# Optimization experiments

Hardware: AMD Instinct MI355X
Metric: run time of the kernel (lower is better)

The kernel has to match this reference:

```python
import jax, jax.numpy as jnp
import numpy as np

B, L, E, H = 4, 4096, 1024, 16
HD = E // H
I = 4096  # intermediate_size = 4*E
RMS_EPS = 1e-6
ATTN_EPS = 1e-6
GATE_INIT = 0.1  # 0.1 + 0.05*layer_idx, layer_idx=0


def rmsnorm(x, w, eps=RMS_EPS):
    xf = x.astype(jnp.float32)
    var = jnp.mean(xf * xf, axis=-1, keepdims=True)
    return w * (xf * jax.lax.rsqrt(var + eps)).astype(x.dtype)


def rotate_half(x):
    d = x.shape[-1] // 2
    return jnp.concatenate([-x[..., d:], x[..., :d]], axis=-1)


def setup_inputs() -> dict:
    key = jax.random.key(0)
    ks = jax.random.split(key, 16)
    h = jax.random.normal(ks[0], (B, L, E), jnp.float32)
    c = jax.random.normal(ks[1], (B, E), jnp.float32)
    # standard RoPE tables, shape (L, HD)
    pos = jnp.arange(L, dtype=jnp.float32)
    inv = 1.0 / (10000.0 ** (jnp.arange(0, HD, 2, dtype=jnp.float32) / HD))
    fr = pos[:, None] * inv[None, :]
    emb = jnp.concatenate([fr, fr], axis=-1)
    cos, sin = jnp.cos(emb), jnp.sin(emb)
    s = 0.02
    Wq = jax.random.normal(ks[2], (E, E), jnp.float32) * s
    Wk = jax.random.normal(ks[3], (E, E), jnp.float32) * s
    Wv = jax.random.normal(ks[4], (E, E), jnp.float32) * s
    Wo = jax.random.normal(ks[5], (E, E), jnp.float32) * s
    Wg = jax.random.normal(ks[6], (I, E), jnp.float32) * s
    Wu = jax.random.normal(ks[7], (I, E), jnp.float32) * s
    Wd = jax.random.normal(ks[8], (E, I), jnp.float32) * s
    w_norm1 = jnp.ones((E,), jnp.float32)
    w_norm2 = jnp.ones((E,), jnp.float32)
    Wada = jax.random.normal(ks[9], (6 * E, E), jnp.float32) * 0.01
    bada = np.zeros((6 * E,), np.float32)
    bada[2 * E:3 * E] = GATE_INIT  # gate_msa
    bada[5 * E:6 * E] = GATE_INIT  # gate_mlp
    bada = jnp.asarray(bada)
    return {"h": h, "c": c, "cos": cos, "sin": sin, "Wq": Wq, "Wk": Wk,
            "Wv": Wv, "Wo": Wo, "Wg": Wg, "Wu": Wu, "Wd": Wd,
            "w_norm1": w_norm1, "w_norm2": w_norm2, "Wada": Wada, "bada": bada}


def reference(h, c, cos, sin, Wq, Wk, Wv, Wo, Wg, Wu, Wd, w_norm1, w_norm2, Wada, bada):
    # adaLN modulation: (B, 6E) -> six (B,1,E) chunks
    mod = c @ Wada.T + bada
    sh1, sc1, g1, sh2, sc2, g2 = [m[:, None, :] for m in jnp.split(mod, 6, axis=-1)]

    # --- attention branch ---
    x = rmsnorm(h, w_norm1) * (1.0 + sc1) + sh1  # modulate
    q = jax.nn.silu(x @ Wq.T).reshape(B, L, H, HD).transpose(0, 2, 1, 3)  # (B,H,L,hd)
    k = jax.nn.silu(x @ Wk.T).reshape(B, L, H, HD).transpose(0, 2, 1, 3)
    v = (x @ Wv.T).reshape(B, L, H, HD).transpose(0, 2, 1, 3)
    cs = cos[None, None]  # (1,1,L,hd)
    sn = sin[None, None]
    q = q * cs + rotate_half(q) * sn
    k = k * cs + rotate_half(k) * sn
    # cosFormer sin/cos feature map; m = max(src,tgt) = L
    idx = (np.pi / 2) * jnp.arange(1, L + 1, dtype=jnp.float32) / L  # (L,)
    sw = jnp.sin(idx)[None, None, :, None]
    cw = jnp.cos(idx)[None, None, :, None]
    q_ = jnp.concatenate([q * sw, q * cw], axis=-1)  # (B,H,L,2hd)
    k_ = jnp.concatenate([k * sw, k * cw], axis=-1)
    # non-causal linear attention: K^T V first (O(L))
    kv = jnp.einsum('bhld,bhlm->bhdm', k_, v)             # (B,H,2hd,hd)
    z = 1.0 / jnp.maximum(jnp.einsum('bhld,bhd->bhl', q_, k_.sum(axis=2)), ATTN_EPS)
    attn = jnp.einsum('bhld,bhdm,bhl->bhlm', q_, kv, z)   # (B,H,L,hd)
    attn = attn.transpose(0, 2, 1, 3).reshape(B, L, E) @ Wo.T
    h = h + g1 * attn  # bias_dropout_add_scale, eval mode

    # --- MLP branch ---
    x = rmsnorm(h, w_norm2) * (1.0 + sc2) + sh2
    mlp = (jax.nn.silu(x @ Wg.T) * (x @ Wu.T)) @ Wd.T
    return h + g2 * mlp
```

## Files before the change

### kernel.cpp

```cpp
#include <hip/hip_runtime.h>
#include <hip/hip_bf16.h>

#define BB 4
#define LL 4096
#define EE 1024
#define HH 16
#define II 4096
#define MM (BB*LL)

using f32x4 = __attribute__((ext_vector_type(4))) float;
using s16x8 = __attribute__((ext_vector_type(8))) short;
using u32x4 = __attribute__((ext_vector_type(4))) unsigned int;

__device__ __forceinline__ unsigned short f2bf(float f) {
  union { float f; unsigned u; } x; x.f = f;
  unsigned r = x.u + 0x7fffu + ((x.u >> 16) & 1u);
  return (unsigned short)(r >> 16);
}
__device__ __forceinline__ float bf2f(unsigned short s) {
  union { unsigned u; float f; } x; x.u = ((unsigned)s) << 16;
  return x.f;
}
__device__ __forceinline__ unsigned packbf(float lo, float hi) {
  return ((unsigned)f2bf(hi) << 16) | (unsigned)f2bf(lo);
}
__device__ __forceinline__ float silu_f(float x) { return x / (1.0f + expf(-x)); }

__device__ __forceinline__ void gll16(const void* g, void* l) {
  __builtin_amdgcn_global_load_lds(
      (const __attribute__((address_space(1))) unsigned int*)g,
      (__attribute__((address_space(3))) unsigned int*)l, 16, 0, 0);
}

__global__ __launch_bounds__(256) void k_mod(const float* __restrict__ c,
    const float* __restrict__ Wada, const float* __restrict__ bada,
    float* __restrict__ mod) {
  __shared__ float cs[EE];
  int b = blockIdx.y;
  int n = blockIdx.x * 256 + threadIdx.x;
  for (int i = threadIdx.x; i < EE; i += 256) cs[i] = c[b*EE + i];
  __syncthreads();
  const float4* wp = (const float4*)(Wada + (size_t)n * EE);
  float acc = 0.f;
  for (int k = 0; k < EE/4; k++) {
    float4 t = wp[k];
    acc += t.x*cs[4*k] + t.y*cs[4*k+1] + t.z*cs[4*k+2] + t.w*cs[4*k+3];
  }
  mod[(size_t)b*6*EE + n] = acc + bada[n];
}

__global__ __launch_bounds__(256) void k_coef(const float* __restrict__ mod,
    const float* __restrict__ w1, const float* __restrict__ w2,
    float* __restrict__ cf1, float* __restrict__ cf2) {
  int k = blockIdx.x * 256 + threadIdx.x;
  int b = blockIdx.y;
  const float* mb = mod + (size_t)b*6*EE;
  cf1[(size_t)b*2048 + k]        = w1[k] * (1.0f + mb[EE + k]);
  cf1[(size_t)b*2048 + 1024 + k] = mb[k];
  cf2[(size_t)b*2048 + k]        = w2[k] * (1.0f + mb[4*EE + k]);
  cf2[(size_t)b*2048 + 1024 + k] = mb[3*EE + k];
}

__global__ __launch_bounds__(256) void k_rsig(const float* __restrict__ in,
    float* __restrict__ rsig) {
  int row = blockIdx.x;
  int t = threadIdx.x;
  float4 v = ((const float4*)(in + (size_t)row * EE))[t];
  float ss = v.x*v.x + v.y*v.y + v.z*v.z + v.w*v.w;
  #pragma unroll
  for (int o = 32; o > 0; o >>= 1) ss += __shfl_down(ss, o, 64);
  __shared__ float red[4];
  if ((t & 63) == 0) red[t >> 6] = ss;
  __syncthreads();
  float tot = red[0] + red[1] + red[2] + red[3];
  if (t == 0) rsig[row] = 1.0f / sqrtf(tot * (1.0f/1024.0f) + 1e-6f);
}

__global__ __launch_bounds__(256) void k_f2b(const float* __restrict__ s,
    unsigned short* __restrict__ d, int n4) {
  int i = blockIdx.x * 256 + threadIdx.x;
  if (i >= n4) return;
  float4 v = ((const float4*)s)[i];
  ushort4 u; u.x = f2bf(v.x); u.y = f2bf(v.y); u.z = f2bf(v.z); u.w = f2bf(v.w);
  ((ushort4*)d)[i] = u;
}

__global__ __launch_bounds__(256) void k_split1(const float* __restrict__ h,
    const float* __restrict__ rsig, const float* __restrict__ cf,
    unsigned short* __restrict__ xh, unsigned short* __restrict__ xl) {
  int row = blockIdx.x;
  int t = threadIdx.x;
  int b = row >> 12;
  float rs = rsig[row];
  const float* cfb = cf + (size_t)b*2048;
  float4 v  = ((const float4*)(h + (size_t)row*EE))[t];
  float4 c1 = ((const float4*)cfb)[t];
  float4 c0 = ((const float4*)(cfb + 1024))[t];
  float x0 = fmaf(v.x*rs, c1.x, c0.x);
  float x1 = fmaf(v.y*rs, c1.y, c0.y);
  float x2 = fmaf(v.z*rs, c1.z, c0.z);
  float x3 = fmaf(v.w*rs, c1.w, c0.w);
  ushort4 uh, ul;
  uh.x = f2bf(x0); ul.x = f2bf(x0 - bf2f(uh.x));
  uh.y = f2bf(x1); ul.y = f2bf(x1 - bf2f(uh.y));
  uh.z = f2bf(x2); ul.z = f2bf(x2 - bf2f(uh.z));
  uh.w = f2bf(x3); ul.w = f2bf(x3 - bf2f(uh.w));
  ((ushort4*)(xh + (size_t)row*EE))[t] = uh;
  ((ushort4*)(xl + (size_t)row*EE))[t] = ul;
}

__global__ __launch_bounds__(256) void k_sgemmK(
    const float* __restrict__ Ah, const float* __restrict__ W,
    const float* __restrict__ rsig, const float* __restrict__ cf,
    const float* __restrict__ cosT, const float* __restrict__ sinT,
    float* __restrict__ outq) {
  __shared__ float As[8][128];
  __shared__ float Bs[8][128];
  __shared__ float c1s[1024];
  __shared__ float c0s[1024];
  int t = threadIdx.x;
  int tx = t & 15, ty = t >> 4;
  int bm = blockIdx.x, bn = blockIdx.y;
  int srow = t >> 1, sk = (t & 1) * 4;
  int bidx = bm >> 5;
  for (int i = t; i < 1024; i += 256) {
    c1s[i] = cf[(size_t)bidx*2048 + i];
    c0s[i] = cf[(size_t)bidx*2048 + 1024 + i];
  }
  int arow = bm*128 + srow;
  float rsA = rsig[arow];
  const float* ap = Ah + (size_t)arow*EE + sk;
  const float* bp = W + (size_t)(bn*128 + srow)*EE + sk;
  float acc[8][8];
  #pragma unroll
  for (int i = 0; i < 8; i++)
    #pragma unroll
    for (int j = 0; j < 8; j++) acc[i][j] = 0.f;
  float4 pa = *(const float4*)ap;
  float4 pb = *(const float4*)bp;
  int c0 = (tx < 8) ? tx*4 : 64 + (tx - 8)*4;
  __syncthreads();
  for (int k0 = 0; k0 < EE; k0 += 8) {
    int kb = k0 + sk;
    As[sk+0][srow] = fmaf(pa.x*rsA, c1s[kb+0], c0s[kb+0]);
    As[sk+1][srow] = fmaf(pa.y*rsA, c1s[kb+1], c0s[kb+1]);
    As[sk+2][srow] = fmaf(pa.z*rsA, c1s[kb+2], c0s[kb+2]);
    As[sk+3][srow] = fmaf(pa.w*rsA, c1s[kb+3], c0s[kb+3]);
    Bs[sk+0][srow] = pb.x; Bs[sk+1][srow] = pb.y; Bs[sk+2][srow] = pb.z; Bs[sk+3][srow] = pb.w;
    __syncthreads();
    if (k0 + 8 < EE) {
      pa = *(const float4*)(ap + k0 + 8);
      pb = *(const float4*)(bp + k0 + 8);
    }
    #pragma unroll
    for (int k = 0; k < 8; k++) {
      float4 a0 = *(const float4*)&As[k][ty*8];
      float4 a1 = *(const float4*)&As[k][ty*8+4];
      float4 b0 = *(const float4*)&Bs[k][c0];
      float4 b1 = *(const float4*)&Bs[k][c0+32];
      float av[8] = {a0.x,a0.y,a0.z,a0.w,a1.x,a1.y,a1.z,a1.w};
      float bv[8]  = {b0.x,b0.y,b0.z,b0.w,b1.x,b1.y,b1.z,b1.w};
      #pragma unroll
      for (int i = 0; i < 8; i++)
        #pragma unroll
        for (int j = 0; j < 8; j++)
          acc[i][j] = fmaf(av[i], bv[j], acc[i][j]);
    }
    __syncthreads();
  }
  int head = bn*2 + (tx >= 8 ? 1 : 0);
  int d0 = (tx < 8) ? tx*4 : (tx - 8)*4;
  #pragma unroll
  for (int i = 0; i < 8; i++) {
    int m = bm*128 + ty*8 + i;
    int b = m >> 12, l = m & 4095;
    const float* cp = cosT + (size_t)l*64;
    const float* sp = sinT + (size_t)l*64;
    float4 cl  = *(const float4*)(cp + d0);
    float4 slv = *(const float4*)(sp + d0);
    float4 chv = *(const float4*)(cp + d0 + 32);
    float4 shv = *(const float4*)(sp + d0 + 32);
    float sA0 = silu_f(acc[i][0]), sA1 = silu_f(acc[i][1]), sA2 = silu_f(acc[i][2]), sA3 = silu_f(acc[i][3]);
    float sB0 = silu_f(acc[i][4]), sB1 = silu_f(acc[i][5]), sB2 = silu_f(acc[i][6]), sB3 = silu_f(acc[i][7]);
    float q00 = sA0*cl.x - sB0*slv.x;
    float q01 = sA1*cl.y - sB1*slv.y;
    float q02 = sA2*cl.z - sB2*slv.z;
    float q03 = sA3*cl.w - sB3*slv.w;
    float q10 = sB0*chv.x + sA0*shv.x;
    float q11 = sB1*chv.y + sA1*shv.y;
    float q12 = sB2*chv.z + sA2*shv.z;
    float q13 = sB3*chv.w + sA3*shv.w;
    float* op = outq + ((size_t)(b*HH + head)*LL + l)*64;
    *(float4*)(op + d0)      = make_float4(q00, q01, q02, q03);
    *(float4*)(op + d0 + 32) = make_float4(q10, q11, q12, q13);
  }
}

__global__ __launch_bounds__(256) void k_qk(
    const unsigned short* __restrict__ xh, const unsigned short* __restrict__ xl,
    const float* __restrict__ W,
    const float* __restrict__ cosT, const float* __restrict__ sinT,
    float* __restrict__ outq) {
  __shared__ unsigned short Ah[128*32];
  __shared__ unsigned short Al[128*32];
  __shared__ unsigned short Bh[64*40];
  __shared__ unsigned short Bl[64*40];
  int t = threadIdx.x, w = t >> 6, lane = t & 63;
  int bm = blockIdx.x, bn = blockIdx.y;
  int wm = (w & 1) * 64;
  int wn = (w >> 1) * 16;
  int r16 = lane & 15, kg = lane >> 4;
  int rin = lane >> 2, slot = lane & 3;
  int ar0 = w*32 + rin, ar1 = ar0 + 16;
  const unsigned short* ahg0 = xh + (size_t)(bm*128 + ar0)*EE + (size_t)((((ar0>>1)&3) ^ slot) * 8);
  const unsigned short* ahg1 = xh + (size_t)(bm*128 + ar1)*EE + (size_t)((((ar1>>1)&3) ^ slot) * 8);
  const unsigned short* alg0 = xl + (size_t)(bm*128 + ar0)*EE + (size_t)((((ar0>>1)&3) ^ slot) * 8);
  const unsigned short* alg1 = xl + (size_t)(bm*128 + ar1)*EE + (size_t)((((ar1>>1)&3) ^ slot) * 8);
  unsigned short* ahl0 = &Ah[(w*32 + 0) * 32];
  unsigned short* ahl1 = &Ah[(w*32 + 16) * 32];
  unsigned short* all0 = &Al[(w*32 + 0) * 32];
  unsigned short* all1 = &Al[(w*32 + 16) * 32];
  int srow = t >> 2, koff = (t & 3) * 8;
  const float* bp = W + (size_t)(bn*64 + srow)*EE + koff;
  float4 pb0 = *(const float4*)(bp + 0);
  float4 pb1 = *(const float4*)(bp + 4);
  f32x4 acc[4][2];
  #pragma unroll
  for (int i = 0; i < 4; i++) { acc[i][0] = (f32x4){0,0,0,0}; acc[i][1] = (f32x4){0,0,0,0}; }

  for (int k0 = 0; k0 < EE; k0 += 32) {
    gll16(ahg0 + k0, ahl0);
    gll16(ahg1 + k0, ahl1);
    gll16(alg0 + k0, all0);
    gll16(alg1 + k0, all1);
    {
      unsigned short h0 = f2bf(pb0.x), h1 = f2bf(pb0.y), h2 = f2bf(pb0.z), h3 = f2bf(pb0.w);
      unsigned short h4 = f2bf(pb1.x), h5 = f2bf(pb1.y), h6 = f2bf(pb1.z), h7 = f2bf(pb1.w);
      unsigned short l0 = f2bf(pb0.x - bf2f(h0)), l1 = f2bf(pb0.y - bf2f(h1));
      unsigned short l2 = f2bf(pb0.z - bf2f(h2)), l3 = f2bf(pb0.w - bf2f(h3));
      unsigned short l4 = f2bf(pb1.x - bf2f(h4)), l5 = f2bf(pb1.y - bf2f(h5));
      unsigned short l6 = f2bf(pb1.z - bf2f(h6)), l7 = f2bf(pb1.w - bf2f(h7));
      u32x4 uh, ul;
      uh[0] = ((unsigned)h1<<16)|h0; uh[1] = ((unsigned)h3<<16)|h2;
      uh[2] = ((unsigned)h5<<16)|h4; uh[3] = ((unsigned)h7<<16)|h6;
      ul[0] = ((unsigned)l1<<16)|l0; ul[1] = ((unsigned)l3<<16)|l2;
      ul[2] = ((unsigned)l5<<16)|l4; ul[3] = ((unsigned)l7<<16)|l6;
      *(u32x4*)&Bh[srow*40 + koff] = uh;
      *(u32x4*)&Bl[srow*40 + koff] = ul;
    }
    __syncthreads();
    if (k0 + 32 < EE) {
      pb0 = *(const float4*)(bp + k0 + 32);
      pb1 = *(const float4*)(bp + k0 + 36);
    }
    int brow0 = wn + r16, brow1 = wn + 32 + r16;
    s16x8 bh0 = *(const s16x8*)&Bh[brow0*40 + kg*8];
    s16x8 bl0 = *(const s16x8*)&Bl[brow0*40 + kg*8];
    s16x8 bh1 = *(const s16x8*)&Bh[brow1*40 + kg*8];
    s16x8 bl1 = *(const s16x8*)&Bl[brow1*40 + kg*8];
    #pragma unroll
    for (int i = 0; i < 4; i++) {
      int row = wm + i*16 + r16;
      int sw = ((((row>>1)&3) ^ kg) << 3);
      s16x8 ah = *(const s16x8*)&Ah[row*32 + sw];
      s16x8 al = *(const s16x8*)&Al[row*32 + sw];
      acc[i][0] = __builtin_amdgcn_mfma_f32_16x16x32_bf16(ah, bh0, acc[i][0], 0, 0, 0);
      acc[i][0] = __builtin_amdgcn_mfma_f32_16x16x32_bf16(ah, bl0, acc[i][0], 0, 0, 0);
      acc[i][0] = __builtin_amdgcn_mfma_f32_16x16x32_bf16(al, bh0, acc[i][0], 0, 0, 0);
      acc[i][1] = __builtin_amdgcn_mfma_f32_16x16x32_bf16(ah, bh1, acc[i][1], 0, 0, 0);
      acc[i][1] = __builtin_amdgcn_mfma_f32_16x16x32_bf16(ah, bl1, acc[i][1], 0, 0, 0);
      acc[i][1] = __builtin_amdgcn_mfma_f32_16x16x32_bf16(al, bh1, acc[i][1], 0, 0, 0);
    }
    __syncthreads();
  }
  int d = wn + r16;
  #pragma unroll
  for (int i = 0; i < 4; i++) {
    #pragma unroll
    for (int r = 0; r < 4; r++) {
      int mm = bm*128 + wm + i*16 + kg*4 + r;
      int b = mm >> 12, l = mm & 4095;
      const float* cp = cosT + (size_t)l*64;
      const float* sp = sinT + (size_t)l*64;
      float sl = silu_f(acc[i][0][r]);
      float sh = silu_f(acc[i][1][r]);
      float qlo = sl*cp[d]      - sh*sp[d];
      float qhi = sh*cp[d + 32] + sl*sp[d + 32];
      float* op = outq + (((size_t)(b*HH + bn))*LL + l)*64;
      op[d]      = qlo;
      op[d + 32] = qhi;
    }
  }
}

template<int EPI, int KD, int AMODE>
__global__ __launch_bounds__(256) void k_gemm2(
    const float* __restrict__ Af, const unsigned short* __restrict__ Ab,
    const unsigned short* __restrict__ Bw,
    const float* __restrict__ rsig, const float* __restrict__ cf,
    const float* __restrict__ res, const float* __restrict__ mod,
    unsigned short* __restrict__ outb, float* __restrict__ outf) {
  constexpr int APAD = (AMODE == 1) ? 40 : 32;
  __shared__ unsigned short As[128 * APAD];
  __shared__ unsigned short Bs[128 * 32];
  __shared__ float c1s[(AMODE == 1) ? 1024 : 1];
  __shared__ float c0s[(AMODE == 1) ? 1024 : 1];
  int t = threadIdx.x, w = t >> 6, lane = t & 63;
  int bm = blockIdx.x, bn = blockIdx.y;
  int wm = (w >> 1) * 64, wn = (w & 1) * 64;
  int rin = lane >> 2, slot = lane & 3;
  int brow0 = w*32 + rin, brow1 = brow0 + 16;
  const unsigned short* bg0 = Bw + (size_t)(bn*128 + brow0)*KD + (size_t)((((brow0>>1)&3) ^ slot) * 8);
  const unsigned short* bg1 = Bw + (size_t)(bn*128 + brow1)*KD + (size_t)((((brow1>>1)&3) ^ slot) * 8);
  unsigned short* bl0 = &Bs[(w*32 + 0) * 32];
  unsigned short* bl1 = &Bs[(w*32 + 16) * 32];
  const unsigned short* ag0 = nullptr; const unsigned short* ag1 = nullptr;
  unsigned short* al0 = nullptr; unsigned short* al1 = nullptr;
  const float* apf = nullptr;
  float rsA = 0.f;
  int srow = t >> 1, koff = (t & 1) * 16;
  float4 ha0, ha1, ha2, ha3;
  if constexpr (AMODE == 1) {
    int bidx = bm >> 5;
    for (int i = t; i < 1024; i += 256) {
      c1s[i] = cf[(size_t)bidx*2048 + i];
      c0s[i] = cf[(size_t)bidx*2048 + 1024 + i];
    }
    rsA = rsig[bm*128 + srow];
    apf = Af + (size_t)(bm*128 + srow)*KD + koff;
    ha0 = *(const float4*)(apf + 0);
    ha1 = *(const float4*)(apf + 4);
    ha2 = *(const float4*)(apf + 8);
    ha3 = *(const float4*)(apf + 12);
    __syncthreads();
  } else {
    ag0 = Ab + (size_t)(bm*128 + brow0)*KD + (size_t)((((brow0>>1)&3) ^ slot) * 8);
    ag1 = Ab + (size_t)(bm*128 + brow1)*KD + (size_t)((((brow1>>1)&3) ^ slot) * 8);
    al0 = &As[(w*32 + 0) * 32];
    al1 = &As[(w*32 + 16) * 32];
  }
  f32x4 acc[4][4];
  #pragma unroll
  for (int i = 0; i < 4; i++)
    #pragma unroll
    for (int j = 0; j < 4; j++) acc[i][j] = (f32x4){0.f, 0.f, 0.f, 0.f};
  int r16 = lane & 15, kg = lane >> 4;
  for (int k0 = 0; k0 < KD; k0 += 32) {
    gll16(bg0 + k0, bl0);
    gll16(bg1 + k0, bl1);
    if constexpr (AMODE == 0) {
      gll16(ag0 + k0, al0);
      gll16(ag1 + k0, al1);
    } else {
      int kb = k0 + koff;
      float x0  = fmaf(ha0.x*rsA, c1s[kb+0],  c0s[kb+0]);
      float x1  = fmaf(ha0.y*rsA, c1s[kb+1],  c0s[kb+1]);
      float x2  = fmaf(ha0.z*rsA, c1s[kb+2],  c0s[kb+2]);
      float x3  = fmaf(ha0.w*rsA, c1s[kb+3],  c0s[kb+3]);
      float x4  = fmaf(ha1.x*rsA, c1s[kb+4],  c0s[kb+4]);
      float x5  = fmaf(ha1.y*rsA, c1s[kb+5],  c0s[kb+5]);
      float x6  = fmaf(ha1.z*rsA, c1s[kb+6],  c0s[kb+6]);
      float x7  = fmaf(ha1.w*rsA, c1s[kb+7],  c0s[kb+7]);
      float x8  = fmaf(ha2.x*rsA, c1s[kb+8],  c0s[kb+8]);
      float x9  = fmaf(ha2.y*rsA, c1s[kb+9],  c0s[kb+9]);
      float x10 = fmaf(ha2.z*rsA, c1s[kb+10], c0s[kb+10]);
      float x11 = fmaf(ha2.w*rsA, c1s[kb+11], c0s[kb+11]);
      float x12 = fmaf(ha3.x*rsA, c1s[kb+12], c0s[kb+12]);
      float x13 = fmaf(ha3.y*rsA, c1s[kb+13], c0s[kb+13]);
      float x14 = fmaf(ha3.z*rsA, c1s[kb+14], c0s[kb+14]);
      float x15 = fmaf(ha3.w*rsA, c1s[kb+15], c0s[kb+15]);
      u32x4 ua, ub;
      ua[0] = packbf(x0, x1);   ua[1] = packbf(x2, x3);
      ua[2] = packbf(x4, x5);   ua[3] = packbf(x6, x7);
      ub[0] = packbf(x8, x9);   ub[1] = packbf(x10, x11);
      ub[2] = packbf(x12, x13); ub[3] = packbf(x14, x15);
      *(u32x4*)&As[srow*APAD + koff]     = ua;
      *(u32x4*)&As[srow*APAD + koff + 8] = ub;
    }
    __syncthreads();
    if constexpr (AMODE == 1) {
      if (k0 + 32 < KD) {
        ha0 = *(const float4*)(apf + k0 + 32);
        ha1 = *(const float4*)(apf + k0 + 36);
        ha2 = *(const float4*)(apf + k0 + 40);
        ha3 = *(const float4*)(apf + k0 + 44);
      }
    }
    s16x8 af[4], bfr[4];
    #pragma unroll
    for (int i = 0; i < 4; i++) {
      int row = wm + i*16 + r16;
      if constexpr (AMODE == 0)
        af[i] = *(const s16x8*)&As[row*32 + ((((row>>1)&3) ^ kg) << 3)];
      else
        af[i] = *(const s16x8*)&As[row*APAD + (kg << 3)];
    }
    #pragma unroll
    for (int j = 0; j < 4; j++) {
      int row = wn + j*16 + r16;
      bfr[j] = *(const s16x8*)&Bs[row*32 + ((((row>>1)&3) ^ kg) << 3)];
    }
    #pragma unroll
    for (int i = 0; i < 4; i++)
      #pragma unroll
      for (int j = 0; j < 4; j++)
        acc[i][j] = __builtin_amdgcn_mfma_f32_16x16x32_bf16(af[i], bfr[j], acc[i][j], 0, 0, 0);
    __syncthreads();
  }
  #pragma unroll
  for (int i = 0; i < 4; i++) {
    #pragma unroll
    for (int j = 0; j < 4; j++) {
      int nn = bn*128 + wn + j*16 + r16;
      #pragma unroll
      for (int r = 0; r < 4; r++) {
        int mm = bm*128 + wm + i*16 + kg*4 + r;
        float v = acc[i][j][r];
        if constexpr (EPI == 0) {
          int b = mm >> 12, l = mm & 4095, hh = nn >> 6, dd = nn & 63;
          outb[(((size_t)(b*HH + hh))*LL + l)*64 + dd] = f2bf(v);
        } else if constexpr (EPI == 1) {
          int b = mm >> 12;
          size_t o = (size_t)mm*EE + nn;
          outf[o] = res[o] + mod[(size_t)b*6*EE + 2*EE + nn] * v;
        } else if constexpr (EPI == 2) {
          outb[(size_t)mm*II + nn] = f2bf(silu_f(v));
        } else if constexpr (EPI == 3) {
          size_t o = (size_t)mm*II + nn;
          outb[o] = f2bf(bf2f(outb[o]) * v);
        } else {
          int b = mm >> 12;
          size_t o = (size_t)mm*EE + nn;
          outf[o] = res[o] + mod[(size_t)b*6*EE + 5*EE + nn] * v;
        }
      }
    }
  }
}

__global__ __launch_bounds__(256) void k_kvpart(const float* __restrict__ kr,
    const unsigned short* __restrict__ vtb, float* __restrict__ kvp) {
  int bi = blockIdx.x;
  int bh = bi >> 3, ch = bi & 7;
  const float* kp = kr + ((size_t)bh*LL + ch*512)*64;
  const unsigned short* vp = vtb + ((size_t)bh*LL + ch*512)*64;
  __shared__ float k8[8][64];
  __shared__ float v8[8][64];
  __shared__ float sw8[8], cw8[8];
  int t = threadIdx.x;
  int d = t >> 2, mq = (t & 3) * 16;
  float accS[16], accC[16];
  #pragma unroll
  for (int q = 0; q < 16; q++) { accS[q] = 0.f; accC[q] = 0.f; }
  float ksS = 0.f, ksC = 0.f;
  for (int l0 = 0; l0 < 512; l0 += 8) {
    __syncthreads();
    #pragma unroll
    for (int rep = 0; rep < 2; rep++) {
      int idx = rep*256 + t;
      k8[idx>>6][idx&63] = kp[(size_t)(l0 + (idx>>6))*64 + (idx&63)];
      v8[idx>>6][idx&63] = bf2f(vp[(size_t)(l0 + (idx>>6))*64 + (idx&63)]);
    }
    if (t < 8) {
      int gl = ch*512 + l0 + t;
      float idxv = 1.5707964f * (float)(gl + 1) * (1.0f/4096.0f);
      sw8[t] = sinf(idxv);
      cw8[t] = cosf(idxv);
    }
    __syncthreads();
    #pragma unroll
    for (int l = 0; l < 8; l++) {
      float kd = k8[l][d];
      float s = kd * sw8[l];
      float c = kd * cw8[l];
      ksS += s; ksC += c;
      const float4* vv = (const float4*)&v8[l][mq];
      #pragma unroll
      for (int q = 0; q < 4; q++) {
        float4 x = vv[q];
        accS[4*q+0] = fmaf(s, x.x, accS[4*q+0]);
        accS[4*q+1] = fmaf(s, x.y, accS[4*q+1]);
        accS[4*q+2] = fmaf(s, x.z, accS[4*q+2]);
        accS[4*q+3] = fmaf(s, x.w, accS[4*q+3]);
        accC[4*q+0] = fmaf(c, x.x, accC[4*q+0]);
        accC[4*q+1] = fmaf(c, x.y, accC[4*q+1]);
        accC[4*q+2] = fmaf(c, x.z, accC[4*q+2]);
        accC[4*q+3] = fmaf(c, x.w, accC[4*q+3]);
      }
    }
  }
  float* op = kvp + (size_t)bi * 8320;
  #pragma unroll
  for (int q = 0; q < 16; q++) {
    op[d*64 + mq + q]        = accS[q];
    op[4096 + d*64 + mq + q] = accC[q];
  }
  if (mq == 0) { op[8192 + d] = ksS; op[8256 + d] = ksC; }
}

__global__ __launch_bounds__(256) void k_kvred(const float* __restrict__ kvp,
    float* __restrict__ kvb) {
  int bh = blockIdx.x;
  for (int i = threadIdx.x; i < 8320; i += 256) {
    float s = 0.f;
    #pragma unroll
    for (int c = 0; c < 8; c++) s += kvp[((size_t)bh*8 + c)*8320 + i];
    kvb[(size_t)bh*8320 + i] = s;
  }
}

__global__ void k_zero(int* __restrict__ cnt) { if (threadIdx.x == 0) *cnt = 0; }

__global__ __launch_bounds__(256) void k_z(const float* __restrict__ qr,
    const float* __restrict__ kvb, float* __restrict__ zb,
    int* __restrict__ list, int* __restrict__ cnt) {
  int bh = blockIdx.x >> 6, lc = blockIdx.x & 63;
  __shared__ float ksS_s[64], ksC_s[64];
  int t = threadIdx.x;
  if (t < 64) ksS_s[t] = kvb[(size_t)bh*8320 + 8192 + t];
  else if (t < 128) ksC_s[t-64] = kvb[(size_t)bh*8320 + 8256 + (t-64)];
  __syncthreads();
  int l = lc*64 + (t >> 2), part = t & 3;
  const float4* qp = (const float4*)(qr + ((size_t)bh*LL + l)*64 + part*16);
  float A = 0.f, Bv = 0.f;
  #pragma unroll
  for (int q = 0; q < 4; q++) {
    float4 x = qp[q];
    int kb = part*16 + 4*q;
    A  += x.x*ksS_s[kb] + x.y*ksS_s[kb+1] + x.z*ksS_s[kb+2] + x.w*ksS_s[kb+3];
    Bv += x.x*ksC_s[kb] + x.y*ksC_s[kb+1] + x.z*ksC_s[kb+2] + x.w*ksC_s[kb+3];
  }
  A  += __shfl_xor(A, 1, 64);  A  += __shfl_xor(A, 2, 64);
  Bv += __shfl_xor(Bv, 1, 64); Bv += __shfl_xor(Bv, 2, 64);
  if (part == 0) {
    float idxv = 1.5707964f * (float)(l + 1) * (1.0f/4096.0f);
    float denom = sinf(idxv)*A + cosf(idxv)*Bv;
    int gid = bh*LL + l;
    zb[gid] = 1.0f / fmaxf(denom, 1e-6f);
    if (fabsf(denom) < 0.05f) {
      int idx = atomicAdd(cnt, 1);
      list[idx] = gid;
    }
  }
}

__global__ __launch_bounds__(256) void k_zfix(const float* __restrict__ h,
    const float* __restrict__ rsig, const float* __restrict__ cf,
    const float* __restrict__ Wq,
    const float* __restrict__ cosT, const float* __restrict__ sinT,
    const float* __restrict__ kvb, const int* __restrict__ list,
    const int* __restrict__ cnt, float* __restrict__ zb) {
  __shared__ float xs[1024];
  __shared__ double qd[64];
  __shared__ double sq[64];
  int n = *cnt;
  int t = threadIdx.x;
  for (int i = blockIdx.x; i < n; i += gridDim.x) {
    int gid = list[i];
    int bh = gid >> 12, l = gid & 4095;
    int b = bh >> 4, hh = bh & 15;
    int row = b*4096 + l;
    float rs = rsig[row];
    const float* cfb = cf + (size_t)b*2048;
    for (int k = t; k < 1024; k += 256)
      xs[k] = fmaf(h[(size_t)row*1024 + k]*rs, cfb[k], cfb[1024 + k]);
    __syncthreads();
    int j = t >> 2, s = t & 3;
    const float* wrow = Wq + (size_t)(hh*64 + j)*1024 + s*256;
    double acc = 0.0;
    for (int k = 0; k < 256; k++)
      acc += (double)wrow[k] * (double)xs[s*256 + k];
    acc += __shfl_xor(acc, 1, 64);
    acc += __shfl_xor(acc, 2, 64);
    if (s == 0) qd[j] = acc;
    __syncthreads();
    if (t < 64) {
      double qv = qd[t];
      sq[t] = qv / (1.0 + exp(-qv));
    }
    __syncthreads();
    if (t == 0) {
      const float* cp = cosT + (size_t)l*64;
      const float* sp = sinT + (size_t)l*64;
      const float* ksS = kvb + (size_t)bh*8320 + 8192;
      const float* ksC = kvb + (size_t)bh*8320 + 8256;
      double dS = 0.0, dC = 0.0;
      for (int d = 0; d < 64; d++) {
        double rot = (d < 32) ? -sq[d + 32] : sq[d - 32];
        double qe = sq[d]*(double)cp[d] + rot*(double)sp[d];
        dS += qe * (double)ksS[d];
        dC += qe * (double)ksC[d];
      }
      double idxv = 1.5707963267948966 * (double)(l + 1) / 4096.0;
      float denom = (float)(sin(idxv)*dS + cos(idxv)*dC);
      zb[gid] = 1.0f / fmaxf(denom, 1e-6f);
    }
    __syncthreads();
  }
}

__global__ __launch_bounds__(256) void k_attn(const float* __restrict__ qr,
    const float* __restrict__ kvb, const float* __restrict__ zb,
    unsigned short* __restrict__ attnb) {
  int bh = blockIdx.x >> 4, lc = blockIdx.x & 15;
  int t = threadIdx.x, w = t >> 6, lane = t & 63;
  const float* kvp_ = kvb + (size_t)bh*8320;
  float kvS[64], kvC[64];
  #pragma unroll
  for (int d = 0; d < 64; d++) kvS[d] = kvp_[d*64 + lane];
  #pragma unroll
  for (int d = 0; d < 64; d++) kvC[d] = kvp_[4096 + d*64 + lane];
  int b = bh >> 4, hh = bh & 15;
  int lbase = lc*256 + w*64;
  for (int li = 0; li < 64; li++) {
    int l = lbase + li;
    const float* qp = qr + ((size_t)bh*LL + l)*64;
    float qv = qp[lane];
    float z = zb[(size_t)bh*LL + l];
    float a0 = 0.f, a1 = 0.f, a2 = 0.f, a3 = 0.f;
    float b0 = 0.f, b1 = 0.f, b2 = 0.f, b3 = 0.f;
    #pragma unroll
    for (int d = 0; d < 64; d += 4) {
      float q0 = __uint_as_float(__builtin_amdgcn_readlane(__float_as_uint(qv), d+0));
      float q1 = __uint_as_float(__builtin_amdgcn_readlane(__float_as_uint(qv), d+1));
      float q2 = __uint_as_float(__builtin_amdgcn_readlane(__float_as_uint(qv), d+2));
      float q3 = __uint_as_float(__builtin_amdgcn_readlane(__float_as_uint(qv), d+3));
      a0 = fmaf(q0, kvS[d+0], a0);
      a1 = fmaf(q1, kvS[d+1], a1);
      a2 = fmaf(q2, kvS[d+2], a2);
      a3 = fmaf(q3, kvS[d+3], a3);
      b0 = fmaf(q0, kvC[d+0], b0);
      b1 = fmaf(q1, kvC[d+1], b1);
      b2 = fmaf(q2, kvC[d+2], b2);
      b3 = fmaf(q3, kvC[d+3], b3);
    }
    float A = (a0 + a1) + (a2 + a3);
    float Bv = (b0 + b1) + (b2 + b3);
    float idxv = 1.5707964f * (float)(l + 1) * (1.0f/4096.0f);
    float num = sinf(idxv)*A + cosf(idxv)*Bv;
    attnb[(((size_t)b*LL + l)*HH + hh)*64 + lane] = f2bf(num * z);
  }
}

extern "C" void kernel_launch(void* const* d_in, const int* in_sizes, int n_in,
                              void* d_out, int out_size, void* d_ws, size_t ws_size,
                              hipStream_t stream) {
  const float* h    = (const float*)d_in[0];
  const float* c    = (const float*)d_in[1];
  const float* cosT = (const float*)d_in[2];
  const float* sinT = (const float*)d_in[3];
  const float* Wq   = (const float*)d_in[4];
  const float* Wk   = (const float*)d_in[5];
  const float* Wv   = (const float*)d_in[6];
  const float* Wo   = (const float*)d_in[7];
  const float* Wg   = (const float*)d_in[8];
  const float* Wu   = (const float*)d_in[9];
  const float* Wd   = (const float*)d_in[10];
  const float* w1   = (const float*)d_in[11];
  const float* w2   = (const float*)d_in[12];
  const float* Wada = (const float*)d_in[13];
  const float* bada = (const float*)d_in[14];
  float* out = (float*)d_out;

  constexpr size_t BIG_SZ   = (size_t)MM * II * 2;
  constexpr size_t WS_NEEDED = BIG_SZ + 131072 + 32768*2 + 65536*2
      + 1048576 + 2129920 + 2097152*2 + 8388608*3;
  if (ws_size < WS_NEEDED) return;

  char* p = (char*)d_ws;
  char* big = p;                               p += BIG_SZ;
  float* mod = (float*)p;                      p += 131072;
  float* cf1 = (float*)p;                      p += 32768;
  float* cf2 = (float*)p;                      p += 32768;
  float* rsig1 = (float*)p;                    p += 65536;
  float* rsig2 = (float*)p;                    p += 65536;
  float* zb  = (float*)p;                      p += 1048576;
  float* kvb = (float*)p;                      p += 2129920;
  unsigned short* Wvb = (unsigned short*)p;    p += 2097152;
  unsigned short* Wob = (unsigned short*)p;    p += 2097152;
  unsigned short* Wgb = (unsigned short*)p;    p += 8388608;
  unsigned short* Wub = (unsigned short*)p;    p += 8388608;
  unsigned short* Wdb = (unsigned short*)p;    p += 8388608;
  unsigned short* xh   = (unsigned short*)big;
  unsigned short* xl   = (unsigned short*)(big + 33554432);
  unsigned short* vtb  = (unsigned short*)(big + 67108864);
  float* kvp           = (float*)(big + 100663296);
  float* qr            = (float*)(big + 67108864);
  int* zf_cnt          = (int*)big;
  int* zf_list         = (int*)(big + 256);
  unsigned short* attnb= (unsigned short*)big;
  unsigned short* Gb   = (unsigned short*)big;
  float* kr            = (float*)d_out;

  k_mod<<<dim3(24, BB), 256, 0, stream>>>(c, Wada, bada, mod);
  k_coef<<<dim3(4, BB), 256, 0, stream>>>(mod, w1, w2, cf1, cf2);
  k_rsig<<<MM, 256, 0, stream>>>(h, rsig1);
  k_f2b<<<1024, 256, 0, stream>>>(Wv, Wvb, EE*EE/4);
  k_f2b<<<1024, 256, 0, stream>>>(Wo, Wob, EE*EE/4);
  k_f2b<<<4096, 256, 0, stream>>>(Wg, Wgb, II*EE/4);
  k_f2b<<<4096, 256, 0, stream>>>(Wu, Wub, II*EE/4);
  k_f2b<<<4096, 256, 0, stream>>>(Wd, Wdb, EE*II/4);
  k_split1<<<MM, 256, 0, stream>>>(h, rsig1, cf1, xh, xl);

  k_sgemmK<<<dim3(128, 8), 256, 0, stream>>>(h, Wk, rsig1, cf1, cosT, sinT, kr);
  k_gemm2<0, EE, 0><<<dim3(128, 8), 256, 0, stream>>>(
      nullptr, xh, Wvb, nullptr, nullptr, nullptr, nullptr, vtb, nullptr);
  k_kvpart<<<BB*HH*8, 256, 0, stream>>>(kr, vtb, kvp);
  k_kvred<<<BB*HH, 256, 0, stream>>>(kvp, kvb);

  k_qk<<<dim3(128, 16), 256, 0, stream>>>(xh, xl, Wq, cosT, sinT, qr);
  k_zero<<<1, 64, 0, stream>>>(zf_cnt);
  k_z<<<BB*HH*(LL/64), 256, 0, stream>>>(qr, kvb, zb, zf_list, zf_cnt);
  k_zfix<<<120, 256, 0, stream>>>(h, rsig1, cf1, Wq, cosT, sinT, kvb,
                                  zf_list, zf_cnt, zb);
  k_attn<<<BB*HH*(LL/256), 256, 0, stream>>>(qr, kvb, zb, attnb);

  k_gemm2<1, EE, 0><<<dim3(128, 8), 256, 0, stream>>>(
      nullptr, attnb, Wob, nullptr, nullptr, h, mod, nullptr, out);

  k_rsig<<<MM, 256, 0, stream>>>(out, rsig2);
  k_gemm2<2, EE, 1><<<dim3(128, 32), 256, 0, stream>>>(
      out, nullptr, Wgb, rsig2, cf2, nullptr, nullptr, Gb, nullptr);
  k_gemm2<3, EE, 1><<<dim3(128, 32), 256, 0, stream>>>(
      out, nullptr, Wub, rsig2, cf2, nullptr, nullptr, Gb, nullptr);
  k_gemm2<4, II, 0><<<dim3(128, 8), 256, 0, stream>>>(
      nullptr, Gb, Wdb, nullptr, nullptr, out, mod, nullptr, out);
}
```

Baseline: 1.854 ms.

## Precompute bf16 modulated MLP input and split MLP into two intermediate halves

Adds a k_split2 kernel that applies the second RMSNorm and modulation once and writes bf16 activations. The gate/up GEMMs then load A tiles with direct global-to-LDS copies instead of recomputing the normalization per N-tile. The MLP is also split into two halves of the intermediate dimension, each running gate, up, then a down-projection over K=2048 that accumulates into the output. This keeps the intermediate buffer at half size, presumably to fit cache better. The cost is an extra pass over the activations and a second read-modify-write of the output in the down GEMM.

New measurement: 1.769 ms. 1.05x faster.

```diff
diff --git a/kernel.cpp b/kernel.cpp
--- a/kernel.cpp
+++ b/kernel.cpp
@@ -20,9 +20,6 @@
 __device__ __forceinline__ float bf2f(unsigned short s) {
   union { unsigned u; float f; } x; x.u = ((unsigned)s) << 16;
   return x.f;
-}
-__device__ __forceinline__ unsigned packbf(float lo, float hi) {
-  return ((unsigned)f2bf(hi) << 16) | (unsigned)f2bf(lo);
 }
 __device__ __forceinline__ float silu_f(float x) { return x / (1.0f + expf(-x)); }
 
@@ -107,6 +104,25 @@
   uh.w = f2bf(x3); ul.w = f2bf(x3 - bf2f(uh.w));
   ((ushort4*)(xh + (size_t)row*EE))[t] = uh;
   ((ushort4*)(xl + (size_t)row*EE))[t] = ul;
+}
+
+__global__ __launch_bounds__(256) void k_split2(const float* __restrict__ in,
+    const float* __restrict__ rsig, const float* __restrict__ cf,
+    unsigned short* __restrict__ xb) {
+  int row = blockIdx.x;
+  int t = threadIdx.x;
+  int b = row >> 12;
+  float rs = rsig[row];
+  const float* cfb = cf + (size_t)b*2048;
+  float4 v  = ((const float4*)(in + (size_t)row*EE))[t];
+  float4 c1 = ((const float4*)cfb)[t];
+  float4 c0 = ((const float4*)(cfb + 1024))[t];
+  ushort4 u;
+  u.x = f2bf(fmaf(v.x*rs, c1.x, c0.x));
+  u.y = f2bf(fmaf(v.y*rs, c1.y, c0.y));
+  u.z = f2bf(fmaf(v.z*rs, c1.z, c0.z));
+  u.w = f2bf(fmaf(v.w*rs, c1.w, c0.w));
+  ((ushort4*)(xb + (size_t)row*EE))[t] = u;
 }
 
 __global__ __launch_bounds__(256) void k_sgemmK(
@@ -293,107 +309,47 @@
   }
 }
 
-template<int EPI, int KD, int AMODE>
+template<int EPI, int KLEN, int SA, int SB>
 __global__ __launch_bounds__(256) void k_gemm2(
-    const float* __restrict__ Af, const unsigned short* __restrict__ Ab,
+    const unsigned short* __restrict__ Ab,
     const unsigned short* __restrict__ Bw,
-    const float* __restrict__ rsig, const float* __restrict__ cf,
+    int kbB, int bnoff,
     const float* __restrict__ res, const float* __restrict__ mod,
     unsigned short* __restrict__ outb, float* __restrict__ outf) {
-  constexpr int APAD = (AMODE == 1) ? 40 : 32;
-  __shared__ unsigned short As[128 * APAD];
+  __shared__ unsigned short As[128 * 32];
   __shared__ unsigned short Bs[128 * 32];
-  __shared__ float c1s[(AMODE == 1) ? 1024 : 1];
-  __shared__ float c0s[(AMODE == 1) ? 1024 : 1];
   int t = threadIdx.x, w = t >> 6, lane = t & 63;
   int bm = blockIdx.x, bn = blockIdx.y;
   int wm = (w >> 1) * 64, wn = (w & 1) * 64;
   int rin = lane >> 2, slot = lane & 3;
   int brow0 = w*32 + rin, brow1 = brow0 + 16;
-  const unsigned short* bg0 = Bw + (size_t)(bn*128 + brow0)*KD + (size_t)((((brow0>>1)&3) ^ slot) * 8);
-  const unsigned short* bg1 = Bw + (size_t)(bn*128 + brow1)*KD + (size_t)((((brow1>>1)&3) ^ slot) * 8);
+  int swz0 = (((brow0>>1)&3) ^ slot) * 8;
+  int swz1 = (((brow1>>1)&3) ^ slot) * 8;
+  const unsigned short* ag0 = Ab + (size_t)(bm*128 + brow0)*SA + swz0;
+  const unsigned short* ag1 = Ab + (size_t)(bm*128 + brow1)*SA + swz1;
+  const unsigned short* bg0 = Bw + (size_t)(bnoff + bn*128 + brow0)*SB + kbB + swz0;
+  const unsigned short* bg1 = Bw + (size_t)(bnoff + bn*128 + brow1)*SB + kbB + swz1;
+  unsigned short* al0 = &As[(w*32 + 0) * 32];
+  unsigned short* al1 = &As[(w*32 + 16) * 32];
   unsigned short* bl0 = &Bs[(w*32 + 0) * 32];
   unsigned short* bl1 = &Bs[(w*32 + 16) * 32];
-  const unsigned short* ag0 = nullptr; const unsigned short* ag1 = nullptr;
-  unsigned short* al0 = nullptr; unsigned short* al1 = nullptr;
-  const float* apf = nullptr;
-  float rsA = 0.f;
-  int srow = t >> 1, koff = (t & 1) * 16;
-  float4 ha0, ha1, ha2, ha3;
-  if constexpr (AMODE == 1) {
-    int bidx = bm >> 5;
-    for (int i = t; i < 1024; i += 256) {
-      c1s[i] = cf[(size_t)bidx*2048 + i];
-      c0s[i] = cf[(size_t)bidx*2048 + 1024 + i];
-    }
-    rsA = rsig[bm*128 + srow];
-    apf = Af + (size_t)(bm*128 + srow)*KD + koff;
-    ha0 = *(const float4*)(apf + 0);
-    ha1 = *(const float4*)(apf + 4);
-    ha2 = *(const float4*)(apf + 8);
-    ha3 = *(const float4*)(apf + 12);
-    __syncthreads();
-  } else {
-    ag0 = Ab + (size_t)(bm*128 + brow0)*KD + (size_t)((((brow0>>1)&3) ^ slot) * 8);
-    ag1 = Ab + (size_t)(bm*128 + brow1)*KD + (size_t)((((brow1>>1)&3) ^ slot) * 8);
-    al0 = &As[(w*32 + 0) * 32];
-    al1 = &As[(w*32 + 16) * 32];
-  }
   f32x4 acc[4][4];
   #pragma unroll
   for (int i = 0; i < 4; i++)
     #pragma unroll
     for (int j = 0; j < 4; j++) acc[i][j] = (f32x4){0.f, 0.f, 0.f, 0.f};
   int r16 = lane & 15, kg = lane >> 4;
-  for (int k0 = 0; k0 < KD; k0 += 32) {
+  for (int k0 = 0; k0 < KLEN; k0 += 32) {
+    gll16(ag0 + k0, al0);
+    gll16(ag1 + k0, al1);
     gll16(bg0 + k0, bl0);
     gll16(bg1 + k0, bl1);
-    if constexpr (AMODE == 0) {
-      gll16(ag0 + k0, al0);
-      gll16(ag1 + k0, al1);
-    } else {
-      int kb = k0 + koff;
-      float x0  = fmaf(ha0.x*rsA, c1s[kb+0],  c0s[kb+0]);
-      float x1  = fmaf(ha0.y*rsA, c1s[kb+1],  c0s[kb+1]);
-      float x2  = fmaf(ha0.z*rsA, c1s[kb+2],  c0s[kb+2]);
-      float x3  = fmaf(ha0.w*rsA, c1s[kb+3],  c0s[kb+3]);
-      float x4  = fmaf(ha1.x*rsA, c1s[kb+4],  c0s[kb+4]);
-      float x5  = fmaf(ha1.y*rsA, c1s[kb+5],  c0s[kb+5]);
-      float x6  = fmaf(ha1.z*rsA, c1s[kb+6],  c0s[kb+6]);
-      float x7  = fmaf(ha1.w*rsA, c1s[kb+7],  c0s[kb+7]);
-      float x8  = fmaf(ha2.x*rsA, c1s[kb+8],  c0s[kb+8]);
-      float x9  = fmaf(ha2.y*rsA, c1s[kb+9],  c0s[kb+9]);
-      float x10 = fmaf(ha2.z*rsA, c1s[kb+10], c0s[kb+10]);
-      float x11 = fmaf(ha2.w*rsA, c1s[kb+11], c0s[kb+11]);
-      float x12 = fmaf(ha3.x*rsA, c1s[kb+12], c0s[kb+12]);
-      float x13 = fmaf(ha3.y*rsA, c1s[kb+13], c0s[kb+13]);
-      float x14 = fmaf(ha3.z*rsA, c1s[kb+14], c0s[kb+14]);
-      float x15 = fmaf(ha3.w*rsA, c1s[kb+15], c0s[kb+15]);
-      u32x4 ua, ub;
-      ua[0] = packbf(x0, x1);   ua[1] = packbf(x2, x3);
-      ua[2] = packbf(x4, x5);   ua[3] = packbf(x6, x7);
-      ub[0] = packbf(x8, x9);   ub[1] = packbf(x10, x11);
-      ub[2] = packbf(x12, x13); ub[3] = packbf(x14, x15);
-      *(u32x4*)&As[srow*APAD + koff]     = ua;
-      *(u32x4*)&As[srow*APAD + koff + 8] = ub;
-    }
-    __syncthreads();
-    if constexpr (AMODE == 1) {
-      if (k0 + 32 < KD) {
-        ha0 = *(const float4*)(apf + k0 + 32);
-        ha1 = *(const float4*)(apf + k0 + 36);
-        ha2 = *(const float4*)(apf + k0 + 40);
-        ha3 = *(const float4*)(apf + k0 + 44);
-      }
-    }
+    __syncthreads();
     s16x8 af[4], bfr[4];
     #pragma unroll
     for (int i = 0; i < 4; i++) {
       int row = wm + i*16 + r16;
-      if constexpr (AMODE == 0)
-        af[i] = *(const s16x8*)&As[row*32 + ((((row>>1)&3) ^ kg) << 3)];
-      else
-        af[i] = *(const s16x8*)&As[row*APAD + (kg << 3)];
+      af[i] = *(const s16x8*)&As[row*32 + ((((row>>1)&3) ^ kg) << 3)];
     }
     #pragma unroll
     for (int j = 0; j < 4; j++) {
@@ -424,9 +380,9 @@
           size_t o = (size_t)mm*EE + nn;
           outf[o] = res[o] + mod[(size_t)b*6*EE + 2*EE + nn] * v;
         } else if constexpr (EPI == 2) {
-          outb[(size_t)mm*II + nn] = f2bf(silu_f(v));
+          outb[(size_t)mm*2048 + nn] = f2bf(silu_f(v));
         } else if constexpr (EPI == 3) {
-          size_t o = (size_t)mm*II + nn;
+          size_t o = (size_t)mm*2048 + nn;
           outb[o] = f2bf(bf2f(outb[o]) * v);
         } else {
           int b = mm >> 12;
@@ -689,7 +645,8 @@
   int* zf_cnt          = (int*)big;
   int* zf_list         = (int*)(big + 256);
   unsigned short* attnb= (unsigned short*)big;
-  unsigned short* Gb   = (unsigned short*)big;
+  unsigned short* x2b  = (unsigned short*)big;
+  unsigned short* Pb   = (unsigned short*)(big + 33554432);
   float* kr            = (float*)d_out;
 
   k_mod<<<dim3(24, BB), 256, 0, stream>>>(c, Wada, bada, mod);
@@ -703,8 +660,8 @@
   k_split1<<<MM, 256, 0, stream>>>(h, rsig1, cf1, xh, xl);
 
   k_sgemmK<<<dim3(128, 8), 256, 0, stream>>>(h, Wk, rsig1, cf1, cosT, sinT, kr);
-  k_gemm2<0, EE, 0><<<dim3(128, 8), 256, 0, stream>>>(
-      nullptr, xh, Wvb, nullptr, nullptr, nullptr, nullptr, vtb, nullptr);
+  k_gemm2<0, EE, EE, EE><<<dim3(128, 8), 256, 0, stream>>>(
+      xh, Wvb, 0, 0, nullptr, nullptr, vtb, nullptr);
   k_kvpart<<<BB*HH*8, 256, 0, stream>>>(kr, vtb, kvp);
   k_kvred<<<BB*HH, 256, 0, stream>>>(kvp, kvb);
 
@@ -715,14 +672,17 @@
                                   zf_list, zf_cnt, zb);
   k_attn<<<BB*HH*(LL/256), 256, 0, stream>>>(qr, kvb, zb, attnb);
 
-  k_gemm2<1, EE, 0><<<dim3(128, 8), 256, 0, stream>>>(
-      nullptr, attnb, Wob, nullptr, nullptr, h, mod, nullptr, out);
+  k_gemm2<1, EE, EE, EE><<<dim3(128, 8), 256, 0, stream>>>(
+      attnb, Wob, 0, 0, h, mod, nullptr, out);
 
   k_rsig<<<MM, 256, 0, stream>>>(out, rsig2);
-  k_gemm2<2, EE, 1><<<dim3(128, 32), 256, 0, stream>>>(
-      out, nullptr, Wgb, rsig2, cf2, nullptr, nullptr, Gb, nullptr);
-  k_gemm2<3, EE, 1><<<dim3(128, 32), 256, 0, stream>>>(
-      out, nullptr, Wub, rsig2, cf2, nullptr, nullptr, Gb, nullptr);
-  k_gemm2<4, II, 0><<<dim3(128, 8), 256, 0, stream>>>(
-      nullptr, Gb, Wdb, nullptr, nullptr, out, mod, nullptr, out);
-}
+  k_split2<<<MM, 256, 0, stream>>>(out, rsig2, cf2, x2b);
+  for (int half = 0; half < 2; half++) {
+    k_gemm2<2, EE, EE, EE><<<dim3(128, 16), 256, 0, stream>>>(
+        x2b, Wgb, 0, half*2048, nullptr, nullptr, Pb, nullptr);
+    k_gemm2<3, EE, EE, EE><<<dim3(128, 16), 256, 0, stream>>>(
+        x2b, Wub, 0, half*2048, nullptr, nullptr, Pb, nullptr);
+    k_gemm2<4, 2048, 2048, II><<<dim3(128, 8), 256, 0, stream>>>(
+        Pb, Wdb, half*2048, 0, out, mod, nullptr, out);
+  }
+}
```
